# Kernel optimization log

Measured on AMD Instinct MI355X. Metric: run time of the kernel, lower is better.

Reference implementation:

```python
import jax, jax.numpy as jnp
import numpy as np


def _gcn_conv(x, W, b, src, dst, num_nodes):
    """PyG GCNConv with default args: add self-loops + symmetric normalization.
    x: [N, F_in], W: [F_in, F_out], b: [F_out], src/dst: [E] (self-loops already included).
    """
    h = x @ W  # [N, F_out]
    # in-degree of destination nodes (counting self-loops)
    ones = jnp.ones_like(dst, dtype=h.dtype)
    deg = jax.ops.segment_sum(ones, dst, num_segments=num_nodes)  # [N]
    dinv = jnp.where(deg > 0, jax.lax.rsqrt(jnp.maximum(deg, 1.0)), 0.0)
    norm = dinv[src] * dinv[dst]  # [E]
    msgs = h[src] * norm[:, None]  # [E, F_out] gather + scale
    out = jax.ops.segment_sum(msgs, dst, num_segments=num_nodes)  # scatter-add
    return out + b


def setup_inputs() -> dict:
    key = jax.random.key(0)
    k1, k2, k3, k4 = jax.random.split(key, 4)
    N, E, F_IN, HID = 100000, 1600000, 128, 64
    x = jax.random.normal(k1, (N, F_IN), dtype=jnp.float32)
    edge_index = jax.random.randint(k2, (2, E), 0, N, dtype=jnp.int64)
    W1 = jax.random.normal(k3, (F_IN, HID), dtype=jnp.float32) * (1.0 / np.sqrt(F_IN))
    b1 = jnp.zeros((HID,), dtype=jnp.float32)
    W2 = jax.random.normal(k4, (HID, 1), dtype=jnp.float32) * (1.0 / np.sqrt(HID))
    b2 = jnp.zeros((1,), dtype=jnp.float32)
    return {"x": x, "edge_index": edge_index, "W1": W1, "b1": b1, "W2": W2, "b2": b2}


def reference(x, edge_index, W1, b1, W2, b2):
    N = x.shape[0]
    # add self-loops (GCNConv default add_self_loops=True)
    loop = jnp.arange(N, dtype=edge_index.dtype)
    src = jnp.concatenate([edge_index[0], loop])
    dst = jnp.concatenate([edge_index[1], loop])
    h = jax.nn.relu(_gcn_conv(x, W1, b1, src, dst, N))
    out = _gcn_conv(h, W2, b2, src, dst, N)
    return out  # [N, 1]
```

## Files before the change

### kernel.cpp

```cpp
#include <hip/hip_runtime.h>
#include <hip/hip_fp16.h>

#define F_IN 128
#define HID  64
#define CAP  96
#define CSHIFT 7
#define CNODES 128
#define NC_MAX 1024
#define CCHUNK 2048
#define BCAPC 2560

typedef short s16x8 __attribute__((ext_vector_type(8)));
typedef float f32x4 __attribute__((ext_vector_type(4)));

__device__ inline unsigned short bf16rne(float f) {
    unsigned u = __float_as_uint(f);
    return (unsigned short)((u + 0x7FFFu + ((u >> 16) & 1u)) >> 16);
}
__device__ inline float bf16tof(unsigned short h) {
    return __uint_as_float(((unsigned)h) << 16);
}

__launch_bounds__(512)
__global__ void k_coarse(const int* __restrict__ src, const int* __restrict__ dst,
                         int* __restrict__ acur, int* __restrict__ ent, int E, int nc,
                         const float* __restrict__ W1, unsigned short* __restrict__ W1hT,
                         unsigned short* __restrict__ W1lT) {
    __shared__ int s_cnt[NC_MAX];
    __shared__ int s_gb[NC_MAX];
    int t = threadIdx.x;

    if (blockIdx.x < 16) {
        int id = blockIdx.x * 512 + t;
        int k = id >> 6, c = id & 63;
        float f = W1[id];
        unsigned short h = bf16rne(f);
        unsigned short l = bf16rne(f - bf16tof(h));
        W1hT[c * F_IN + k] = h;
        W1lT[c * F_IN + k] = l;
    }

    int e0 = blockIdx.x * CCHUNK;

    for (int i = t; i < nc; i += 512) { s_cnt[i] = 0; }
    __syncthreads();

    int d0 = 0, d1 = 0, d2 = 0, d3 = 0, s0 = 0, s1 = 0, s2 = 0, s3 = 0;
    int n = E - e0;
    bool v0 = (t          < n), v1 = (t + 512  < n),
         v2 = (t + 1024   < n), v3 = (t + 1536 < n);
    if (v0) { d0 = dst[e0 + t];          s0 = src[e0 + t]; }
    if (v1) { d1 = dst[e0 + t + 512];    s1 = src[e0 + t + 512]; }
    if (v2) { d2 = dst[e0 + t + 1024];   s2 = src[e0 + t + 1024]; }
    if (v3) { d3 = dst[e0 + t + 1536];   s3 = src[e0 + t + 1536]; }

    if (v0) atomicAdd(&s_cnt[d0 >> CSHIFT], 1);
    if (v1) atomicAdd(&s_cnt[d1 >> CSHIFT], 1);
    if (v2) atomicAdd(&s_cnt[d2 >> CSHIFT], 1);
    if (v3) atomicAdd(&s_cnt[d3 >> CSHIFT], 1);
    __syncthreads();

    for (int i = t; i < nc; i += 512) {
        int c = s_cnt[i];
        s_gb[i] = (c > 0) ? atomicAdd(&acur[i], c) : 0;
    }
    __syncthreads();

    if (v0) { int b = d0 >> CSHIFT; int p = atomicAdd(&s_gb[b], 1);
              if (p < BCAPC) ent[(size_t)b * BCAPC + p] = (s0 << CSHIFT) | (d0 & (CNODES - 1)); }
    if (v1) { int b = d1 >> CSHIFT; int p = atomicAdd(&s_gb[b], 1);
              if (p < BCAPC) ent[(size_t)b * BCAPC + p] = (s1 << CSHIFT) | (d1 & (CNODES - 1)); }
    if (v2) { int b = d2 >> CSHIFT; int p = atomicAdd(&s_gb[b], 1);
              if (p < BCAPC) ent[(size_t)b * BCAPC + p] = (s2 << CSHIFT) | (d2 & (CNODES - 1)); }
    if (v3) { int b = d3 >> CSHIFT; int p = atomicAdd(&s_gb[b], 1);
              if (p < BCAPC) ent[(size_t)b * BCAPC + p] = (s3 << CSHIFT) | (d3 & (CNODES - 1)); }
}

__launch_bounds__(1024)
__global__ void k_fillc(const int* __restrict__ acur, const int* __restrict__ ent,
                        int* __restrict__ counts, int* __restrict__ csrc, int N) {
    __shared__ int lcnt[CNODES];
    int b = blockIdx.x, t = threadIdx.x;
    if (t < CNODES) lcnt[t] = 0;
    __syncthreads();
    int base = b * CNODES;
    int cnt = acur[b]; if (cnt > BCAPC) cnt = BCAPC;
    const int* ep = ent + (size_t)b * BCAPC;
    for (int i = t; i < cnt; i += 1024) {
        int v = ep[i];
        int ld = v & (CNODES - 1), s = v >> CSHIFT;
        int p = atomicAdd(&lcnt[ld], 1);
        if (p < CAP) csrc[(size_t)(base + ld) * CAP + p] = s;
    }
    __syncthreads();
    if (t < CNODES && base + t < N) {
        int cc = lcnt[t]; if (cc > CAP) cc = CAP;
        counts[base + t] = cc;
    }
}

__launch_bounds__(256)
__global__ void k_gemm(const float* __restrict__ x,
                       const unsigned short* __restrict__ W1hT,
                       const unsigned short* __restrict__ W1lT,
                       const int* __restrict__ counts, __half* __restrict__ hn, int N) {
    int t = threadIdx.x;
    int lane = t & 63;
    int wid = t >> 6;
    int r0w = blockIdx.x * 64 + wid * 16;
    int arow = r0w + (lane & 15);
    int ar = (arow < N) ? arow : (N - 1);
    int kq = lane >> 4;

    const float* xr = x + (size_t)ar * F_IN + kq * 8;
    int coff = (lane & 15) * F_IN + kq * 8;

    f32x4 acc[4];
#pragma unroll
    for (int nt = 0; nt < 4; ++nt) acc[nt] = (f32x4){0.f, 0.f, 0.f, 0.f};

#pragma unroll
    for (int kt = 0; kt < 4; ++kt) {
        float4 xa = *(const float4*)(xr + kt * 32);
        float4 xb = *(const float4*)(xr + kt * 32 + 4);
        float xf[8] = {xa.x, xa.y, xa.z, xa.w, xb.x, xb.y, xb.z, xb.w};
        s16x8 ah, al;
#pragma unroll
        for (int j = 0; j < 8; ++j) {
            unsigned short h = bf16rne(xf[j]);
            ah[j] = (short)h;
            al[j] = (short)bf16rne(xf[j] - bf16tof(h));
        }
        int kb = coff + kt * 32;
#pragma unroll
        for (int nt = 0; nt < 4; ++nt) {
            s16x8 bh = *(const s16x8*)(W1hT + nt * 16 * F_IN + kb);
            s16x8 bl = *(const s16x8*)(W1lT + nt * 16 * F_IN + kb);
            acc[nt] = __builtin_amdgcn_mfma_f32_16x16x32_bf16(ah, bh, acc[nt], 0, 0, 0);
            acc[nt] = __builtin_amdgcn_mfma_f32_16x16x32_bf16(al, bh, acc[nt], 0, 0, 0);
            acc[nt] = __builtin_amdgcn_mfma_f32_16x16x32_bf16(ah, bl, acc[nt], 0, 0, 0);
            acc[nt] = __builtin_amdgcn_mfma_f32_16x16x32_bf16(al, bl, acc[nt], 0, 0, 0);
        }
    }

    int rbase = r0w + (lane >> 4) * 4;
    if (rbase >= N) return;
    int4 c4 = *(const int4*)(counts + rbase);
    int cj[4] = {c4.x, c4.y, c4.z, c4.w};
#pragma unroll
    for (int j = 0; j < 4; ++j) {
        int row = rbase + j;
        if (row < N) {
            float di = rsqrtf((float)(cj[j] + 1));
            __half* hp = hn + (size_t)row * HID + (lane & 15);
#pragma unroll
            for (int nt = 0; nt < 4; ++nt)
                hp[nt * 16] = __float2half_rn(acc[nt][j] * di);
        }
    }
}

__device__ inline void accum8(float acc[8], int4 raw, float w) {
    int v[4] = { raw.x, raw.y, raw.z, raw.w };
#pragma unroll
    for (int h = 0; h < 4; ++h) {
        __half2 h2 = *(__half2*)&v[h];
        float2 f = __half22float2(h2);
        acc[2 * h]     = fmaf(w, f.x, acc[2 * h]);
        acc[2 * h + 1] = fmaf(w, f.y, acc[2 * h + 1]);
    }
}

__launch_bounds__(256)
__global__ void k_gather1(const int* __restrict__ csrc, const int* __restrict__ counts,
                          const __half* __restrict__ hn, const float* __restrict__ b1,
                          const float* __restrict__ W2, float* __restrict__ zn, int N) {
    int lane = threadIdx.x & 63;
    int g    = (lane >> 3) & 3;
    int li   = lane & 7;
    int r = blockIdx.x * 8 + ((threadIdx.x >> 6) << 1) + (lane >> 5);
    int rr = (r < N) ? r : (N - 1);
    int cnt = (r < N) ? counts[rr] : 0;

    const int4* cs4 = (const int4*)(csrc + (size_t)rr * CAP);
    size_t lo = (size_t)li * 8;

    float acc[8];
#pragma unroll
    for (int c = 0; c < 8; ++c) acc[c] = 0.f;

    {
        int4 sA = cs4[g];
        int idx[4]; float w[4];
        idx[0] = sA.x; idx[1] = sA.y; idx[2] = sA.z; idx[3] = sA.w;
#pragma unroll
        for (int k = 0; k < 4; ++k) {
            int e = 4 * g + k;
            bool v = (e < cnt);
            idx[k] = v ? idx[k] : rr;
            w[k]   = v ? 1.f : 0.f;
        }
        int4 raw[4];
#pragma unroll
        for (int k = 0; k < 4; ++k)
            raw[k] = *(const int4*)&hn[(size_t)idx[k] * HID + lo];
#pragma unroll
        for (int k = 0; k < 4; ++k) accum8(acc, raw[k], w[k]);
    }

    int cntO = __shfl_xor(cnt, 32, 64);
    int cmax = (cnt > cntO) ? cnt : cntO;

    if (cmax > 16) {
        int4 sB = cs4[4 + g];
        int idx[4]; float w[4];
        idx[0] = sB.x; idx[1] = sB.y; idx[2] = sB.z; idx[3] = sB.w;
#pragma unroll
        for (int k = 0; k < 4; ++k) {
            int e = 16 + 4 * g + k;
            bool v = (e < cnt);
            idx[k] = v ? idx[k] : rr;
            w[k]   = v ? 1.f : 0.f;
        }
        int4 raw[4];
#pragma unroll
        for (int k = 0; k < 4; ++k)
            raw[k] = *(const int4*)&hn[(size_t)idx[k] * HID + lo];
#pragma unroll
        for (int k = 0; k < 4; ++k) accum8(acc, raw[k], w[k]);
    }

    for (int c = 32; c < cmax; c += 16) {
        int4 s = cs4[(c >> 2) + g];
        int idx[4]; float w[4];
        idx[0] = s.x; idx[1] = s.y; idx[2] = s.z; idx[3] = s.w;
#pragma unroll
        for (int k = 0; k < 4; ++k) {
            int e = c + 4 * g + k;
            bool v = (e < cnt);
            idx[k] = v ? idx[k] : rr;
            w[k]   = v ? 1.f : 0.f;
        }
        int4 raw[4];
#pragma unroll
        for (int k = 0; k < 4; ++k)
            raw[k] = *(const int4*)&hn[(size_t)idx[k] * HID + lo];
#pragma unroll
        for (int k = 0; k < 4; ++k) accum8(acc, raw[k], w[k]);
    }

#pragma unroll
    for (int c = 0; c < 8; ++c) {
        acc[c] += __shfl_xor(acc[c], 8, 64);
        acc[c] += __shfl_xor(acc[c], 16, 64);
    }

    int4 rawR = *(const int4*)&hn[(size_t)rr * HID + lo];
    accum8(acc, rawR, 1.f);

    float di = rsqrtf((float)(cnt + 1));
    float4 b0 = *(const float4*)&b1[li * 8];
    float4 b4 = *(const float4*)&b1[li * 8 + 4];
    float4 w0 = *(const float4*)&W2[li * 8];
    float4 w4 = *(const float4*)&W2[li * 8 + 4];

    float p = fmaxf(fmaf(di, acc[0], b0.x), 0.f) * w0.x
            + fmaxf(fmaf(di, acc[1], b0.y), 0.f) * w0.y
            + fmaxf(fmaf(di, acc[2], b0.z), 0.f) * w0.z
            + fmaxf(fmaf(di, acc[3], b0.w), 0.f) * w0.w
            + fmaxf(fmaf(di, acc[4], b4.x), 0.f) * w4.x
            + fmaxf(fmaf(di, acc[5], b4.y), 0.f) * w4.y
            + fmaxf(fmaf(di, acc[6], b4.z), 0.f) * w4.z
            + fmaxf(fmaf(di, acc[7], b4.w), 0.f) * w4.w;

    p += __shfl_xor(p, 1, 64);
    p += __shfl_xor(p, 2, 64);
    p += __shfl_xor(p, 4, 64);

    if ((lane & 31) == 0 && r < N) zn[r] = p * di;
}

__global__ void k_gather2(const int* __restrict__ csrc, const int* __restrict__ counts,
                          const float* __restrict__ zn, const float* __restrict__ b2,
                          float* __restrict__ out, int N) {
    int t = blockIdx.x * blockDim.x + threadIdx.x;
    int r = t >> 4, li = t & 15;
    if (r >= N) return;
    size_t beg = (size_t)r * CAP;
    int cnt = counts[r];
    float acc = 0.f;
    for (int j = li; j < cnt; j += 16) {
        acc += zn[csrc[beg + j]];
    }
    acc += __shfl_xor(acc, 1, 64);
    acc += __shfl_xor(acc, 2, 64);
    acc += __shfl_xor(acc, 4, 64);
    acc += __shfl_xor(acc, 8, 64);
    if (li == 0) {
        float di = rsqrtf((float)(cnt + 1));
        out[r] = di * (acc + zn[r]) + b2[0];
    }
}

extern "C" void kernel_launch(void* const* d_in, const int* in_sizes, int n_in,
                              void* d_out, int out_size, void* d_ws, size_t ws_size,
                              hipStream_t stream) {
    const float* x  = (const float*)d_in[0];
    const int*   ei = (const int*)d_in[1];
    const float* W1 = (const float*)d_in[2];
    const float* b1 = (const float*)d_in[3];
    const float* W2 = (const float*)d_in[4];
    const float* b2 = (const float*)d_in[5];
    float* out = (float*)d_out;

    const int N = in_sizes[0] / F_IN;
    const int E = in_sizes[1] / 2;
    const int* src = ei;
    const int* dst = ei + E;

    const int nc = (N + CNODES - 1) / CNODES;
    const int NBKT = (N + 63) / 64;

    char* ws = (char*)d_ws;
    size_t off = 0;
    auto alloc = [&](size_t bytes) { void* p = ws + off; off += (bytes + 255) & ~255ULL; return p; };
    int*    acur   = (int*)   alloc((size_t)nc * 4);
    int*    counts = (int*)   alloc((size_t)N * 4);
    float*  zn     = (float*) alloc((size_t)N * 4);
    unsigned short* W1hT = (unsigned short*) alloc((size_t)HID * F_IN * 2);
    unsigned short* W1lT = (unsigned short*) alloc((size_t)HID * F_IN * 2);
    int*    ent    = (int*)   alloc((size_t)nc * BCAPC * 4);
    __half* hn     = (__half*)alloc((size_t)N * HID * 2);
    int*    csrc   = (int*)   alloc((size_t)N * CAP * 4);

    hipMemsetAsync(acur, 0, (size_t)nc * 4, stream);

    const int coarseBlks = (E + CCHUNK - 1) / CCHUNK;
    k_coarse<<<coarseBlks, 512, 0, stream>>>(src, dst, acur, ent, E, nc, W1, W1hT, W1lT);
    k_fillc<<<nc, 1024, 0, stream>>>(acur, ent, counts, csrc, N);
    k_gemm<<<NBKT, 256, 0, stream>>>(x, W1hT, W1lT, counts, hn, N);
    k_gather1<<<(N + 7) / 8, 256, 0, stream>>>(csrc, counts, hn, b1, W2, zn, N);
    k_gather2<<<((size_t)N * 16 + 255) / 256, 256, 0, stream>>>(csrc, counts, zn, b2, out, N);
}
```

Before: 207.6 us.

## Fuse CSR fill into gather kernel via shared-memory bucket lists

Removes the k_fillc pass and the global csrc array. Per-node counts now come from global atomics in the coarse bucketing kernel, and the layer-1 gather rebuilds each 128-node bucket's adjacency in shared memory before aggregating. Layer 2 becomes a bucket-wise scatter with shared-memory float atomics over the entry list. The W1 split moves into its own tiny kernel. This avoids writing and re-reading the large padded CSR array, at the cost of global atomics on counts, low occupancy from a 48KB shared-memory 1024-thread block with only ~782 blocks, and a counts value that is no longer capped at CAP.

Result: slower. 265.2 us (+27.7%).

```diff
diff --git a/kernel.cpp b/kernel.cpp
--- a/kernel.cpp
+++ b/kernel.cpp
@@ -22,37 +22,42 @@
 }
 
 __launch_bounds__(512)
+__global__ void k_wsplit(const float* __restrict__ W1, unsigned short* __restrict__ W1hT,
+                         unsigned short* __restrict__ W1lT) {
+    int id = blockIdx.x * 512 + threadIdx.x;
+    int k = id >> 6, c = id & 63;
+    float f = W1[id];
+    unsigned short h = bf16rne(f);
+    unsigned short l = bf16rne(f - bf16tof(h));
+    W1hT[c * F_IN + k] = h;
+    W1lT[c * F_IN + k] = l;
+}
+
+__launch_bounds__(512)
 __global__ void k_coarse(const int* __restrict__ src, const int* __restrict__ dst,
-                         int* __restrict__ acur, int* __restrict__ ent, int E, int nc,
-                         const float* __restrict__ W1, unsigned short* __restrict__ W1hT,
-                         unsigned short* __restrict__ W1lT) {
+                         int* __restrict__ acur, int* __restrict__ counts,
+                         int* __restrict__ ent, int E, int nc) {
     __shared__ int s_cnt[NC_MAX];
     __shared__ int s_gb[NC_MAX];
     int t = threadIdx.x;
-
-    if (blockIdx.x < 16) {
-        int id = blockIdx.x * 512 + t;
-        int k = id >> 6, c = id & 63;
-        float f = W1[id];
-        unsigned short h = bf16rne(f);
-        unsigned short l = bf16rne(f - bf16tof(h));
-        W1hT[c * F_IN + k] = h;
-        W1lT[c * F_IN + k] = l;
-    }
-
     int e0 = blockIdx.x * CCHUNK;
 
-    for (int i = t; i < nc; i += 512) { s_cnt[i] = 0; }
+    for (int i = t; i < nc; i += 512) s_cnt[i] = 0;
     __syncthreads();
 
     int d0 = 0, d1 = 0, d2 = 0, d3 = 0, s0 = 0, s1 = 0, s2 = 0, s3 = 0;
     int n = E - e0;
-    bool v0 = (t          < n), v1 = (t + 512  < n),
-         v2 = (t + 1024   < n), v3 = (t + 1536 < n);
-    if (v0) { d0 = dst[e0 + t];          s0 = src[e0 + t]; }
-    if (v1) { d1 = dst[e0 + t + 512];    s1 = src[e0 + t + 512]; }
-    if (v2) { d2 = dst[e0 + t + 1024];   s2 = src[e0 + t + 1024]; }
-    if (v3) { d3 = dst[e0 + t + 1536];   s3 = src[e0 + t + 1536]; }
+    bool v0 = (t        < n), v1 = (t + 512  < n),
+         v2 = (t + 1024 < n), v3 = (t + 1536 < n);
+    if (v0) { d0 = dst[e0 + t];        s0 = src[e0 + t]; }
+    if (v1) { d1 = dst[e0 + t + 512];  s1 = src[e0 + t + 512]; }
+    if (v2) { d2 = dst[e0 + t + 1024]; s2 = src[e0 + t + 1024]; }
+    if (v3) { d3 = dst[e0 + t + 1536]; s3 = src[e0 + t + 1536]; }
+
+    if (v0) atomicAdd(&counts[d0], 1);
+    if (v1) atomicAdd(&counts[d1], 1);
+    if (v2) atomicAdd(&counts[d2], 1);
+    if (v3) atomicAdd(&counts[d3], 1);
 
     if (v0) atomicAdd(&s_cnt[d0 >> CSHIFT], 1);
     if (v1) atomicAdd(&s_cnt[d1 >> CSHIFT], 1);
@@ -74,29 +79,6 @@
               if (p < BCAPC) ent[(size_t)b * BCAPC + p] = (s2 << CSHIFT) | (d2 & (CNODES - 1)); }
     if (v3) { int b = d3 >> CSHIFT; int p = atomicAdd(&s_gb[b], 1);
               if (p < BCAPC) ent[(size_t)b * BCAPC + p] = (s3 << CSHIFT) | (d3 & (CNODES - 1)); }
-}
-
-__launch_bounds__(1024)
-__global__ void k_fillc(const int* __restrict__ acur, const int* __restrict__ ent,
-                        int* __restrict__ counts, int* __restrict__ csrc, int N) {
-    __shared__ int lcnt[CNODES];
-    int b = blockIdx.x, t = threadIdx.x;
-    if (t < CNODES) lcnt[t] = 0;
-    __syncthreads();
-    int base = b * CNODES;
-    int cnt = acur[b]; if (cnt > BCAPC) cnt = BCAPC;
-    const int* ep = ent + (size_t)b * BCAPC;
-    for (int i = t; i < cnt; i += 1024) {
-        int v = ep[i];
-        int ld = v & (CNODES - 1), s = v >> CSHIFT;
-        int p = atomicAdd(&lcnt[ld], 1);
-        if (p < CAP) csrc[(size_t)(base + ld) * CAP + p] = s;
-    }
-    __syncthreads();
-    if (t < CNODES && base + t < N) {
-        int cc = lcnt[t]; if (cc > CAP) cc = CAP;
-        counts[base + t] = cc;
-    }
 }
 
 __launch_bounds__(256)
@@ -171,134 +153,160 @@
     }
 }
 
-__launch_bounds__(256)
-__global__ void k_gather1(const int* __restrict__ csrc, const int* __restrict__ counts,
-                          const __half* __restrict__ hn, const float* __restrict__ b1,
-                          const float* __restrict__ W2, float* __restrict__ zn, int N) {
-    int lane = threadIdx.x & 63;
+__launch_bounds__(1024)
+__global__ void k_fg1(const int* __restrict__ acur, const int* __restrict__ ent,
+                      const __half* __restrict__ hn, const float* __restrict__ b1,
+                      const float* __restrict__ W2, float* __restrict__ zn, int N) {
+    __shared__ int lcnt[CNODES];
+    __shared__ int csrcL[CNODES * CAP];
+    int b = blockIdx.x, t = threadIdx.x;
+    if (t < CNODES) lcnt[t] = 0;
+    __syncthreads();
+
+    int base = b * CNODES;
+    int cnt_b = acur[b]; if (cnt_b > BCAPC) cnt_b = BCAPC;
+    const int* ep = ent + (size_t)b * BCAPC;
+    for (int i = t; i < cnt_b; i += 1024) {
+        int v = ep[i];
+        int ld = v & (CNODES - 1), s = v >> CSHIFT;
+        int p = atomicAdd(&lcnt[ld], 1);
+        if (p < CAP) csrcL[ld * CAP + p] = s;
+    }
+    __syncthreads();
+
+    int lane = t & 63;
     int g    = (lane >> 3) & 3;
     int li   = lane & 7;
-    int r = blockIdx.x * 8 + ((threadIdx.x >> 6) << 1) + (lane >> 5);
-    int rr = (r < N) ? r : (N - 1);
-    int cnt = (r < N) ? counts[rr] : 0;
-
-    const int4* cs4 = (const int4*)(csrc + (size_t)rr * CAP);
+    int wv   = t >> 6;
     size_t lo = (size_t)li * 8;
 
-    float acc[8];
-#pragma unroll
-    for (int c = 0; c < 8; ++c) acc[c] = 0.f;
-
-    {
-        int4 sA = cs4[g];
-        int idx[4]; float w[4];
-        idx[0] = sA.x; idx[1] = sA.y; idx[2] = sA.z; idx[3] = sA.w;
-#pragma unroll
-        for (int k = 0; k < 4; ++k) {
-            int e = 4 * g + k;
-            bool v = (e < cnt);
-            idx[k] = v ? idx[k] : rr;
-            w[k]   = v ? 1.f : 0.f;
-        }
-        int4 raw[4];
-#pragma unroll
-        for (int k = 0; k < 4; ++k)
-            raw[k] = *(const int4*)&hn[(size_t)idx[k] * HID + lo];
-#pragma unroll
-        for (int k = 0; k < 4; ++k) accum8(acc, raw[k], w[k]);
-    }
-
-    int cntO = __shfl_xor(cnt, 32, 64);
-    int cmax = (cnt > cntO) ? cnt : cntO;
-
-    if (cmax > 16) {
-        int4 sB = cs4[4 + g];
-        int idx[4]; float w[4];
-        idx[0] = sB.x; idx[1] = sB.y; idx[2] = sB.z; idx[3] = sB.w;
-#pragma unroll
-        for (int k = 0; k < 4; ++k) {
-            int e = 16 + 4 * g + k;
-            bool v = (e < cnt);
-            idx[k] = v ? idx[k] : rr;
-            w[k]   = v ? 1.f : 0.f;
-        }
-        int4 raw[4];
-#pragma unroll
-        for (int k = 0; k < 4; ++k)
-            raw[k] = *(const int4*)&hn[(size_t)idx[k] * HID + lo];
-#pragma unroll
-        for (int k = 0; k < 4; ++k) accum8(acc, raw[k], w[k]);
-    }
-
-    for (int c = 32; c < cmax; c += 16) {
-        int4 s = cs4[(c >> 2) + g];
-        int idx[4]; float w[4];
-        idx[0] = s.x; idx[1] = s.y; idx[2] = s.z; idx[3] = s.w;
-#pragma unroll
-        for (int k = 0; k < 4; ++k) {
-            int e = c + 4 * g + k;
-            bool v = (e < cnt);
-            idx[k] = v ? idx[k] : rr;
-            w[k]   = v ? 1.f : 0.f;
-        }
-        int4 raw[4];
-#pragma unroll
-        for (int k = 0; k < 4; ++k)
-            raw[k] = *(const int4*)&hn[(size_t)idx[k] * HID + lo];
-#pragma unroll
-        for (int k = 0; k < 4; ++k) accum8(acc, raw[k], w[k]);
-    }
-
-#pragma unroll
-    for (int c = 0; c < 8; ++c) {
-        acc[c] += __shfl_xor(acc[c], 8, 64);
-        acc[c] += __shfl_xor(acc[c], 16, 64);
-    }
-
-    int4 rawR = *(const int4*)&hn[(size_t)rr * HID + lo];
-    accum8(acc, rawR, 1.f);
-
-    float di = rsqrtf((float)(cnt + 1));
     float4 b0 = *(const float4*)&b1[li * 8];
     float4 b4 = *(const float4*)&b1[li * 8 + 4];
     float4 w0 = *(const float4*)&W2[li * 8];
     float4 w4 = *(const float4*)&W2[li * 8 + 4];
 
-    float p = fmaxf(fmaf(di, acc[0], b0.x), 0.f) * w0.x
-            + fmaxf(fmaf(di, acc[1], b0.y), 0.f) * w0.y
-            + fmaxf(fmaf(di, acc[2], b0.z), 0.f) * w0.z
-            + fmaxf(fmaf(di, acc[3], b0.w), 0.f) * w0.w
-            + fmaxf(fmaf(di, acc[4], b4.x), 0.f) * w4.x
-            + fmaxf(fmaf(di, acc[5], b4.y), 0.f) * w4.y
-            + fmaxf(fmaf(di, acc[6], b4.z), 0.f) * w4.z
-            + fmaxf(fmaf(di, acc[7], b4.w), 0.f) * w4.w;
-
-    p += __shfl_xor(p, 1, 64);
-    p += __shfl_xor(p, 2, 64);
-    p += __shfl_xor(p, 4, 64);
-
-    if ((lane & 31) == 0 && r < N) zn[r] = p * di;
-}
-
-__global__ void k_gather2(const int* __restrict__ csrc, const int* __restrict__ counts,
-                          const float* __restrict__ zn, const float* __restrict__ b2,
-                          float* __restrict__ out, int N) {
-    int t = blockIdx.x * blockDim.x + threadIdx.x;
-    int r = t >> 4, li = t & 15;
-    if (r >= N) return;
-    size_t beg = (size_t)r * CAP;
-    int cnt = counts[r];
-    float acc = 0.f;
-    for (int j = li; j < cnt; j += 16) {
-        acc += zn[csrc[beg + j]];
-    }
-    acc += __shfl_xor(acc, 1, 64);
-    acc += __shfl_xor(acc, 2, 64);
-    acc += __shfl_xor(acc, 4, 64);
-    acc += __shfl_xor(acc, 8, 64);
-    if (li == 0) {
+#pragma unroll
+    for (int pass = 0; pass < 4; ++pass) {
+        int ld = pass * 32 + wv * 2 + (lane >> 5);
+        int r  = base + ld;
+        int rr = (r < N) ? r : (N - 1);
+        int cnt = (r < N) ? lcnt[ld] : 0;
+        int cw  = (cnt > CAP) ? CAP : cnt;
+        const int4* cs4 = (const int4*)&csrcL[ld * CAP];
+
+        float acc[8];
+#pragma unroll
+        for (int c = 0; c < 8; ++c) acc[c] = 0.f;
+
+        {
+            int4 sA = cs4[g];
+            int idx[4]; float w[4];
+            idx[0] = sA.x; idx[1] = sA.y; idx[2] = sA.z; idx[3] = sA.w;
+#pragma unroll
+            for (int k = 0; k < 4; ++k) {
+                int e = 4 * g + k;
+                bool v = (e < cw);
+                idx[k] = v ? idx[k] : rr;
+                w[k]   = v ? 1.f : 0.f;
+            }
+            int4 raw[4];
+#pragma unroll
+            for (int k = 0; k < 4; ++k)
+                raw[k] = *(const int4*)&hn[(size_t)idx[k] * HID + lo];
+#pragma unroll
+            for (int k = 0; k < 4; ++k) accum8(acc, raw[k], w[k]);
+        }
+
+        int cntO = __shfl_xor(cw, 32, 64);
+        int cmax = (cw > cntO) ? cw : cntO;
+
+        if (cmax > 16) {
+            int4 sB = cs4[4 + g];
+            int idx[4]; float w[4];
+            idx[0] = sB.x; idx[1] = sB.y; idx[2] = sB.z; idx[3] = sB.w;
+#pragma unroll
+            for (int k = 0; k < 4; ++k) {
+                int e = 16 + 4 * g + k;
+                bool v = (e < cw);
+                idx[k] = v ? idx[k] : rr;
+                w[k]   = v ? 1.f : 0.f;
+            }
+            int4 raw[4];
+#pragma unroll
+            for (int k = 0; k < 4; ++k)
+                raw[k] = *(const int4*)&hn[(size_t)idx[k] * HID + lo];
+#pragma unroll
+            for (int k = 0; k < 4; ++k) accum8(acc, raw[k], w[k]);
+        }
+
+        for (int c = 32; c < cmax; c += 16) {
+            int4 s = cs4[(c >> 2) + g];
+            int idx[4]; float w[4];
+            idx[0] = s.x; idx[1] = s.y; idx[2] = s.z; idx[3] = s.w;
+#pragma unroll
+            for (int k = 0; k < 4; ++k) {
+                int e = c + 4 * g + k;
+                bool v = (e < cw);
+                idx[k] = v ? idx[k] : rr;
+                w[k]   = v ? 1.f : 0.f;
+            }
+            int4 raw[4];
+#pragma unroll
+            for (int k = 0; k < 4; ++k)
+                raw[k] = *(const int4*)&hn[(size_t)idx[k] * HID + lo];
+#pragma unroll
+            for (int k = 0; k < 4; ++k) accum8(acc, raw[k], w[k]);
+        }
+
+#pragma unroll
+        for (int c = 0; c < 8; ++c) {
+            acc[c] += __shfl_xor(acc[c], 8, 64);
+            acc[c] += __shfl_xor(acc[c], 16, 64);
+        }
+
+        int4 rawR = *(const int4*)&hn[(size_t)rr * HID + lo];
+        accum8(acc, rawR, 1.f);
+
         float di = rsqrtf((float)(cnt + 1));
-        out[r] = di * (acc + zn[r]) + b2[0];
+        float p = fmaxf(fmaf(di, acc[0], b0.x), 0.f) * w0.x
+                + fmaxf(fmaf(di, acc[1], b0.y), 0.f) * w0.y
+                + fmaxf(fmaf(di, acc[2], b0.z), 0.f) * w0.z
+                + fmaxf(fmaf(di, acc[3], b0.w), 0.f) * w0.w
+                + fmaxf(fmaf(di, acc[4], b4.x), 0.f) * w4.x
+                + fmaxf(fmaf(di, acc[5], b4.y), 0.f) * w4.y
+                + fmaxf(fmaf(di, acc[6], b4.z), 0.f) * w4.z
+                + fmaxf(fmaf(di, acc[7], b4.w), 0.f) * w4.w;
+
+        p += __shfl_xor(p, 1, 64);
+        p += __shfl_xor(p, 2, 64);
+        p += __shfl_xor(p, 4, 64);
+
+        if ((lane & 31) == 0 && r < N) zn[r] = p * di;
+    }
+}
+
+__launch_bounds__(256)
+__global__ void k_g2e(const int* __restrict__ acur, const int* __restrict__ ent,
+                      const int* __restrict__ counts, const float* __restrict__ zn,
+                      const float* __restrict__ b2, float* __restrict__ out, int N) {
+    __shared__ float accum[CNODES];
+    int b = blockIdx.x, t = threadIdx.x;
+    if (t < CNODES) accum[t] = 0.f;
+    __syncthreads();
+    int base = b * CNODES;
+    int cnt_b = acur[b]; if (cnt_b > BCAPC) cnt_b = BCAPC;
+    const int* ep = ent + (size_t)b * BCAPC;
+    for (int i = t; i < cnt_b; i += 256) {
+        int v = ep[i];
+        atomicAdd(&accum[v & (CNODES - 1)], zn[v >> CSHIFT]);
+    }
+    __syncthreads();
+    if (t < CNODES) {
+        int node = base + t;
+        if (node < N) {
+            float di = rsqrtf((float)(counts[node] + 1));
+            out[node] = di * (accum[t] + zn[node]) + b2[0];
+        }
     }
 }
 
@@ -325,20 +333,20 @@
     size_t off = 0;
     auto alloc = [&](size_t bytes) { void* p = ws + off; off += (bytes + 255) & ~255ULL; return p; };
     int*    acur   = (int*)   alloc((size_t)nc * 4);
-    int*    counts = (int*)   alloc((size_t)N * 4);
+    int*    counts = (int*)   alloc((size_t)N * 4 + 256);
     float*  zn     = (float*) alloc((size_t)N * 4);
     unsigned short* W1hT = (unsigned short*) alloc((size_t)HID * F_IN * 2);
     unsigned short* W1lT = (unsigned short*) alloc((size_t)HID * F_IN * 2);
     int*    ent    = (int*)   alloc((size_t)nc * BCAPC * 4);
     __half* hn     = (__half*)alloc((size_t)N * HID * 2);
-    int*    csrc   = (int*)   alloc((size_t)N * CAP * 4);
-
-    hipMemsetAsync(acur, 0, (size_t)nc * 4, stream);
+
+    size_t zspan = (size_t)((char*)counts - (char*)acur) + (size_t)N * 4;
+    hipMemsetAsync(acur, 0, zspan, stream);
 
     const int coarseBlks = (E + CCHUNK - 1) / CCHUNK;
-    k_coarse<<<coarseBlks, 512, 0, stream>>>(src, dst, acur, ent, E, nc, W1, W1hT, W1lT);
-    k_fillc<<<nc, 1024, 0, stream>>>(acur, ent, counts, csrc, N);
+    k_wsplit<<<16, 512, 0, stream>>>(W1, W1hT, W1lT);
+    k_coarse<<<coarseBlks, 512, 0, stream>>>(src, dst, acur, counts, ent, E, nc);
     k_gemm<<<NBKT, 256, 0, stream>>>(x, W1hT, W1lT, counts, hn, N);
-    k_gather1<<<(N + 7) / 8, 256, 0, stream>>>(csrc, counts, hn, b1, W2, zn, N);
-    k_gather2<<<((size_t)N * 16 + 255) / 256, 256, 0, stream>>>(csrc, counts, zn, b2, out, N);
-}
+    k_fg1<<<nc, 1024, 0, stream>>>(acur, ent, hn, b1, W2, zn, N);
+    k_g2e<<<nc, 256, 0, stream>>>(acur, ent, counts, zn, b2, out, N);
+}
```
